# Kernel optimization log

Measured on AMD Instinct MI355X. Metric: run time of the kernel, lower is better.

## Reference

```python
import jax, jax.numpy as jnp
import numpy as np

S = 1.0   # scale s
M = 0.4   # margin m
EPS = 1e-12  # F.normalize eps


def _l2norm_rows(a):
    # F.normalize(a, dim=1): row-wise L2 normalization
    n = jnp.linalg.norm(a, axis=1, keepdims=True)
    return a / jnp.maximum(n, EPS)


def _half_loss(sim):
    # unique-label branch: positive is the diagonal, all off-diagonal are negatives
    N = sim.shape[0]
    num = S * (jnp.diagonal(sim) - M)                       # [N]
    offdiag = jnp.exp(S * sim) * (1.0 - jnp.eye(N, dtype=sim.dtype))
    denom = jnp.exp(num) + jnp.sum(offdiag, axis=1)         # [N]
    return num - jnp.log(denom)


def setup_inputs() -> dict:
    key = jax.random.key(0)
    k1, k2 = jax.random.split(key)
    N, D = 8192, 256
    return {
        "x1": jax.random.normal(k1, (N, D), dtype=jnp.float32),
        "x2": jax.random.normal(k2, (N, D), dtype=jnp.float32),
        "sentence_id": jnp.arange(N, dtype=jnp.int32),  # unique labels -> more_label=False branch
    }


def reference(x1, x2, sentence_id):
    # x12[i,j] row-normalized similarity of x1_i against all x2_j (and symmetric)
    x12 = _l2norm_rows(x1 @ x2.T)   # [N, N]
    x21 = _l2norm_rows(x2 @ x1.T)   # [N, N]
    L12 = _half_loss(x12)
    L21 = _half_loss(x21)
    loss = -jnp.mean(L12) - jnp.mean(L21)
    return loss, L12, L21
```

## Files before the change

kernel.cpp:

```cpp
#include <hip/hip_runtime.h>
#include <cstdint>
#include <cstddef>


#define NROWS 8192
#define DIMK 256
#define MARGIN 0.4f
#define LOG2E 1.4426950408889634f
#define LN2 0.6931471805599453f

typedef short short8 __attribute__((ext_vector_type(8)));
typedef float f32x4 __attribute__((ext_vector_type(4)));
typedef long longx2 __attribute__((ext_vector_type(2)));

__device__ __forceinline__ unsigned short f2bf(float f) {
  union { float f; unsigned u; } v; v.f = f;
  unsigned r = (v.u + 0x7fffu + ((v.u >> 16) & 1u)) >> 16;
  return (unsigned short)r;
}

__device__ __forceinline__ unsigned char f2fp8(float f) {
  union { float f; unsigned u; } v; v.f = f;
  const unsigned s = (v.u >> 24) & 0x80u;
  const unsigned au = v.u & 0x7fffffffu;
  if (au >= 0x43e00000u) return (unsigned char)(s | 0x7eu);
  int e = (int)(au >> 23) - 127;
  if (e >= -6) {
    unsigned mfull = (au & 0x7fffffu) | 0x800000u;
    unsigned r = (mfull + 0x7ffffu + ((mfull >> 20) & 1u)) >> 20;
    if (r == 16u) { r = 8u; ++e; }
    return (unsigned char)(s | ((unsigned)(e + 7) << 3) | (r & 7u));
  }
  float scaled = __builtin_fabsf(f) * 512.0f;
  unsigned n = (unsigned)(scaled + 0.5f);
  if (n >= 8u) return (unsigned char)(s | 0x08u);
  return (unsigned char)(s | n);
}

__device__ __forceinline__ void gl_lds16(const void* g, void* l) {
  __builtin_amdgcn_global_load_lds((const __attribute__((address_space(1))) void*)g,
                                   (__attribute__((address_space(3))) void*)l, 16, 0, 0);
}

__device__ __forceinline__ float fexp(float x) {
  return __builtin_amdgcn_exp2f(x * LOG2E);
}

__global__ __launch_bounds__(256)
void k_prep(const float* __restrict__ x1, const float* __restrict__ x2,
            unsigned short* __restrict__ Ab, unsigned short* __restrict__ Bb,
            unsigned char* __restrict__ A8, unsigned char* __restrict__ B8,
            float* __restrict__ diag, float* __restrict__ zero_region) {
  const int t = threadIdx.x;
  if (blockIdx.x < 2048) {
    const int row = blockIdx.x * 4 + (t >> 6);
    const int l = t & 63;
    const float4 a = ((const float4*)(x1 + (size_t)row * DIMK))[l];
    const float4 b = ((const float4*)(x2 + (size_t)row * DIMK))[l];
    ushort4 ua, ub;
    ua.x = f2bf(a.x); ua.y = f2bf(a.y); ua.z = f2bf(a.z); ua.w = f2bf(a.w);
    ub.x = f2bf(b.x); ub.y = f2bf(b.y); ub.z = f2bf(b.z); ub.w = f2bf(b.w);
    ((ushort4*)(Ab + (size_t)row * DIMK))[l] = ua;
    ((ushort4*)(Bb + (size_t)row * DIMK))[l] = ub;
    uchar4 qa, qb;
    qa.x = f2fp8(a.x); qa.y = f2fp8(a.y); qa.z = f2fp8(a.z); qa.w = f2fp8(a.w);
    qb.x = f2fp8(b.x); qb.y = f2fp8(b.y); qb.z = f2fp8(b.z); qb.w = f2fp8(b.w);
    ((uchar4*)(A8 + (size_t)row * DIMK))[l] = qa;
    ((uchar4*)(B8 + (size_t)row * DIMK))[l] = qb;
    float d = a.x * b.x + a.y * b.y + a.z * b.z + a.w * b.w;
#pragma unroll
    for (int m = 1; m < 64; m <<= 1) d += __shfl_xor(d, m);
    if (l == 0) diag[row] = d;
  } else {
    const size_t off = (size_t)(blockIdx.x - 2048) * 1024 + t * 4;
    float4 z = {0.f, 0.f, 0.f, 0.f};
    *(float4*)(zero_region + off) = z;
  }
}

__global__ __launch_bounds__(256)
void k_syrk(const unsigned short* __restrict__ Ab, const unsigned short* __restrict__ Bb,
            float* __restrict__ M1, float* __restrict__ M2) {
  __shared__ unsigned short As[64 * 32];
  __shared__ unsigned short Bs[64 * 32];
  const int t = threadIdx.x, w = t >> 6, l = t & 63, quad = l >> 4, l15 = l & 15;
  const int mat = blockIdx.z & 1;
  const int kseg = blockIdx.z >> 1;
  const unsigned short* X = mat ? Bb : Ab;
  float* Mo = mat ? M2 : M1;
  const int a0 = blockIdx.y * 64, b0 = blockIdx.x * 64;
  const int wr = (w >> 1) * 32, wc = (w & 1) * 32;
  f32x4 acc[2][2] = {};
  const int nn = t & 31, cb = t >> 5;
  const int c0 = cb * 8;
  const int nb = kseg * 256;
  for (int n0 = nb; n0 < nb + 256; n0 += 32) {
    short8 va = *(const short8*)(X + (size_t)(n0 + nn) * DIMK + a0 + c0);
    short8 vb = *(const short8*)(X + (size_t)(n0 + nn) * DIMK + b0 + c0);
#pragma unroll
    for (int i = 0; i < 8; ++i) {
      const int c = c0 + i;
      const int sl = (((nn >> 3) ^ ((c >> 1) & 3)) << 3) + (nn & 7);
      As[c * 32 + sl] = va[i];
      Bs[c * 32 + sl] = vb[i];
    }
    __syncthreads();
    short8 af[2], bg[2];
#pragma unroll
    for (int i = 0; i < 2; ++i) {
      const int ra = wr + i * 16 + l15;
      af[i] = *(const short8*)&As[ra * 32 + ((quad ^ ((ra >> 1) & 3)) << 3)];
      const int rb = wc + i * 16 + l15;
      bg[i] = *(const short8*)&Bs[rb * 32 + ((quad ^ ((rb >> 1) & 3)) << 3)];
    }
#pragma unroll
    for (int i = 0; i < 2; ++i)
#pragma unroll
      for (int j = 0; j < 2; ++j)
        acc[i][j] = __builtin_amdgcn_mfma_f32_16x16x32_bf16(af[i], bg[j], acc[i][j], 0, 0, 0);
    __syncthreads();
  }
#pragma unroll
  for (int i = 0; i < 2; ++i)
#pragma unroll
    for (int j = 0; j < 2; ++j)
#pragma unroll
      for (int r = 0; r < 4; ++r) {
        const int lr = wr + i * 16 + quad * 4 + r;
        const int lc = wc + j * 16 + l15;
        atomicAdd(&Mo[(size_t)(a0 + lr) * 256 + b0 + lc], acc[i][j][r]);
      }
}

__global__ __launch_bounds__(256)
void k_gemmN(const unsigned short* __restrict__ Ab, const unsigned short* __restrict__ Bb,
             const float* __restrict__ M1, const float* __restrict__ M2,
             const float* __restrict__ x1, const float* __restrict__ x2,
             float* __restrict__ rowsq, float* __restrict__ colsq) {
  __shared__ unsigned short As[2][4096];
  __shared__ unsigned short Bs[2][4096];
  const int t = threadIdx.x, w = t >> 6, l = t & 63, quad = l >> 4, l15 = l & 15;
  const unsigned short* A;
  const float* Mf;
  const float* Xf;
  float* sq;
  if ((blockIdx.z & 1) == 0) { A = Ab; Mf = M2; Xf = x1; sq = rowsq; }
  else                       { A = Bb; Mf = M1; Xf = x2; sq = colsq; }
  const int kbase = (blockIdx.z >> 1) * 128;
  const int row0 = blockIdx.x * 128;
  const int col0 = blockIdx.y * 128;
  const int wr = (w >> 1) * 64, wc = (w & 1) * 64;
  f32x4 acc[4][4] = {};

  const int sr0 = l >> 2, slot = l & 3;
  const int cA = w * 2, cB = w * 2 + 1;
  const int rA = cA * 16 + sr0, rB = cB * 16 + sr0;
  const int scA = (slot ^ ((rA >> 1) & 3)) << 3;
  const int scB = (slot ^ ((rB >> 1) & 3)) << 3;
  const unsigned short* pA0 = A + (size_t)(row0 + rA) * DIMK + kbase + scA;
  const unsigned short* pA1 = A + (size_t)(row0 + rB) * DIMK + kbase + scB;
  const int dA0 = cA * 512 + l * 8, dA1 = cB * 512 + l * 8;

  auto stageB = [&](int k0, int buf) {
#pragma unroll
    for (int g = 0; g < 2; ++g) {
      const int e = g * 2048 + t * 8;
      const int c = e >> 5, kk = e & 31;
      const float4 v0 = *(const float4*)(Mf + (size_t)(col0 + c) * 256 + kbase + k0 + kk);
      const float4 v1 = *(const float4*)(Mf + (size_t)(col0 + c) * 256 + kbase + k0 + kk + 4);
      ushort4 u0, u1;
      u0.x = f2bf(v0.x); u0.y = f2bf(v0.y); u0.z = f2bf(v0.z); u0.w = f2bf(v0.w);
      u1.x = f2bf(v1.x); u1.y = f2bf(v1.y); u1.z = f2bf(v1.z); u1.w = f2bf(v1.w);
      const int sw = ((kk >> 3) ^ ((c >> 1) & 3)) << 3;
      *(ushort4*)&Bs[buf][c * 32 + sw] = u0;
      *(ushort4*)&Bs[buf][c * 32 + sw + 4] = u1;
    }
  };
  auto issueA = [&](int k0, int buf) {
    gl_lds16(pA0 + k0, &As[buf][dA0]);
    gl_lds16(pA1 + k0, &As[buf][dA1]);
  };

  stageB(0, 0);
  issueA(0, 0);
#pragma unroll
  for (int k = 0; k < 4; ++k) {
    const int cur = k & 1;
    __syncthreads();
    if (k < 3) { stageB((k + 1) * 32, cur ^ 1); issueA((k + 1) * 32, cur ^ 1); }
    short8 af[4], bg[4];
#pragma unroll
    for (int i = 0; i < 4; ++i) {
      const int ra = wr + i * 16 + l15;
      af[i] = *(const short8*)&As[cur][ra * 32 + ((quad ^ ((ra >> 1) & 3)) << 3)];
      const int rb = wc + i * 16 + l15;
      bg[i] = *(const short8*)&Bs[cur][rb * 32 + ((quad ^ ((rb >> 1) & 3)) << 3)];
    }
#pragma unroll
    for (int i = 0; i < 4; ++i)
#pragma unroll
      for (int j = 0; j < 4; ++j)
        acc[i][j] = __builtin_amdgcn_mfma_f32_16x16x32_bf16(af[i], bg[j], acc[i][j], 0, 0, 0);
  }

#pragma unroll
  for (int i = 0; i < 4; ++i) {
#pragma unroll
    for (int r = 0; r < 4; ++r) {
      const int lr = wr + i * 16 + quad * 4 + r;
      const float* xr = Xf + (size_t)(row0 + lr) * DIMK + col0 + wc;
      float rp = 0.f;
#pragma unroll
      for (int j = 0; j < 4; ++j) rp += acc[i][j][r] * xr[j * 16 + l15];
      rp += __shfl_xor(rp, 1); rp += __shfl_xor(rp, 2);
      rp += __shfl_xor(rp, 4); rp += __shfl_xor(rp, 8);
      if (l15 == 0) atomicAdd(&sq[row0 + lr], rp);
    }
  }
}

__global__ __launch_bounds__(256)
void k_gemmE(const unsigned char* __restrict__ A8, const unsigned char* __restrict__ B8,
             const float* __restrict__ rowsq, const float* __restrict__ colsq,
             float* __restrict__ rowExp, float* __restrict__ colExp) {
  __shared__ unsigned char As[2][8192];
  __shared__ unsigned char Bs[2][8192];
  __shared__ float cRow[128];
  __shared__ float cCol[128];

  const int t = threadIdx.x;
  const int w = t >> 6;
  const int l = t & 63;
  const int quad = l >> 4;
  const int l15 = l & 15;
  const int row0 = blockIdx.x * 128;
  const int col0 = blockIdx.y * 128;
  const int wr = (w >> 1) * 64;
  const int wc = (w & 1) * 64;

  if (t < 128) cRow[t] = LOG2E * rsqrtf(rowsq[row0 + t]);
  else cCol[t - 128] = LOG2E * rsqrtf(colsq[col0 + t - 128]);

  f32x4 acc[4][4] = {};

  const int srow = t >> 2;
  const int cl = (t & 3) ^ ((t >> 3) & 3);
  const unsigned char* gA0 = A8 + (size_t)(row0 + srow) * DIMK + cl * 16;
  const unsigned char* gA1 = A8 + (size_t)(row0 + 64 + srow) * DIMK + cl * 16;
  const unsigned char* gB0 = B8 + (size_t)(col0 + srow) * DIMK + cl * 16;
  const unsigned char* gB1 = B8 + (size_t)(col0 + 64 + srow) * DIMK + cl * 16;
  const int d0 = t * 16, d1 = 4096 + t * 16;

  auto issue = [&](int k0, int buf) {
    gl_lds16(gA0 + k0, &As[buf][d0]);
    gl_lds16(gA1 + k0, &As[buf][d1]);
    gl_lds16(gB0 + k0, &Bs[buf][d0]);
    gl_lds16(gB1 + k0, &Bs[buf][d1]);
  };

  issue(0, 0);
#pragma unroll
  for (int it = 0; it < 4; ++it) {
    const int cur = it & 1;
    __syncthreads();
    if (it < 3) issue((it + 1) * 64, cur ^ 1);
    longx2 av[4], bv[4];
#pragma unroll
    for (int i = 0; i < 4; ++i) {
      const int ra = wr + i * 16 + l15;
      const int pcA = quad ^ ((ra >> 1) & 3);
      av[i] = *(const longx2*)&As[cur][ra * 64 + pcA * 16];
      const int rb = wc + i * 16 + l15;
      const int pcB = quad ^ ((rb >> 1) & 3);
      bv[i] = *(const longx2*)&Bs[cur][rb * 64 + pcB * 16];
    }
#pragma unroll
    for (int kc = 0; kc < 2; ++kc)
#pragma unroll
      for (int i = 0; i < 4; ++i)
#pragma unroll
        for (int j = 0; j < 4; ++j)
          acc[i][j] = __builtin_amdgcn_mfma_f32_16x16x32_fp8_fp8(av[i][kc], bv[j][kc],
                                                                 acc[i][j], 0, 0, 0);
  }

  float cj[4];
#pragma unroll
  for (int j = 0; j < 4; ++j) cj[j] = cCol[wc + j * 16 + l15];
  float colpart[4] = {0.f, 0.f, 0.f, 0.f};
#pragma unroll
  for (int i = 0; i < 4; ++i) {
#pragma unroll
    for (int r = 0; r < 4; ++r) {
      const int lr = wr + i * 16 + quad * 4 + r;
      const float ci = cRow[lr];
      float rp = 0.f;
#pragma unroll
      for (int j = 0; j < 4; ++j) {
        const float g = acc[i][j][r];
        rp += __builtin_amdgcn_exp2f(g * ci);
        colpart[j] += __builtin_amdgcn_exp2f(g * cj[j]);
      }
      rp += __shfl_xor(rp, 1); rp += __shfl_xor(rp, 2);
      rp += __shfl_xor(rp, 4); rp += __shfl_xor(rp, 8);
      if (l15 == 0) atomicAdd(&rowExp[row0 + lr], rp);
    }
  }
#pragma unroll
  for (int j = 0; j < 4; ++j) {
    float cp = colpart[j];
    cp += __shfl_xor(cp, 16); cp += __shfl_xor(cp, 32);
    if (l < 16) atomicAdd(&colExp[col0 + wc + j * 16 + l15], cp);
  }
}

__global__ __launch_bounds__(1024)
void k_final(const float* __restrict__ rowsq, const float* __restrict__ colsq,
             const float* __restrict__ diag, const float* __restrict__ rowExp,
             const float* __restrict__ colExp, float* __restrict__ out,
             double* __restrict__ lossAcc, int* __restrict__ doneCnt) {
  const int t = threadIdx.x;
  const int i = blockIdx.x * 1024 + t;
  const float d = diag[i];
  const float s1 = d * rsqrtf(rowsq[i]);
  const float s2 = d * rsqrtf(colsq[i]);
  const float n1 = s1 - MARGIN, n2 = s2 - MARGIN;
  const float L1 = n1 - LN2 * __builtin_amdgcn_logf(rowExp[i] - fexp(s1) + fexp(n1));
  const float L2 = n2 - LN2 * __builtin_amdgcn_logf(colExp[i] - fexp(s2) + fexp(n2));
  out[1 + i] = L1;
  out[1 + NROWS + i] = L2;
  double part = (double)L1 + (double)L2;
#pragma unroll
  for (int m = 1; m < 64; m <<= 1) part += __shfl_xor(part, m);
  __shared__ double red[16];
  if ((t & 63) == 0) red[t >> 6] = part;
  __syncthreads();
  if (t == 0) {
    double s = 0.0;
#pragma unroll
    for (int q = 0; q < 16; ++q) s += red[q];
    atomicAdd(lossAcc, s);
    __threadfence();
    if (atomicAdd(doneCnt, 1) == 7) {
      const double la =
          __hip_atomic_load(lossAcc, __ATOMIC_ACQUIRE, __HIP_MEMORY_SCOPE_AGENT);
      out[0] = (float)(-la / (double)NROWS);
    }
  }
}

extern "C" void kernel_launch(void* const* d_in, const int* in_sizes, int n_in,
                              void* d_out, int out_size, void* d_ws, size_t ws_size,
                              hipStream_t stream) {
  const float* x1 = (const float*)d_in[0];
  const float* x2 = (const float*)d_in[1];
  float* out = (float*)d_out;
  char* ws = (char*)d_ws;

  unsigned short* Ab = (unsigned short*)(ws);
  unsigned short* Bb = (unsigned short*)(ws + 4194304);
  float* M1 = (float*)(ws + 8388608);
  float* M2 = (float*)(ws + 8650752);
  float* rowsq = (float*)(ws + 8912896);
  float* colsq = (float*)(ws + 8945664);
  float* rowExp = (float*)(ws + 8978432);
  float* colExp = (float*)(ws + 9011200);
  char* ctrl = ws + 9043968;
  double* lossAcc = (double*)(ctrl);
  int* doneCnt = (int*)(ctrl + 256);
  float* diag = (float*)(ws + 9048064);
  unsigned char* A8 = (unsigned char*)(ws + 9080832);
  unsigned char* B8 = (unsigned char*)(ws + 11177984);

  k_prep<<<2209, 256, 0, stream>>>(x1, x2, Ab, Bb, A8, B8, diag,
                                   (float*)(ws + 8388608));
  k_syrk<<<dim3(4, 4, 64), 256, 0, stream>>>(Ab, Bb, M1, M2);
  k_gemmN<<<dim3(64, 2, 4), 256, 0, stream>>>(Ab, Bb, M1, M2, x1, x2, rowsq, colsq);
  k_gemmE<<<dim3(64, 64), 256, 0, stream>>>(A8, B8, rowsq, colsq, rowExp, colExp);
  k_final<<<8, 1024, 0, stream>>>(rowsq, colsq, diag, rowExp, colExp, out,
                                  lossAcc, doneCnt);
}
```

Before: 170.9 us.

## Fuse all five kernels into one persistent cooperative kernel with grid syncs

Merges the prep, SYRK, norm GEMM, fp8 exp GEMM and final reduction kernels into a single cooperative persistent kernel. Each phase loops over virtual block indices, and grid-wide syncs separate the phases, which removes four kernel launch boundaries and the done-counter handshake. The trade-offs are a shared LDS footprint sized for the largest phase, which may reduce occupancy, plus grid.sync costs and less latency hiding in the GEMM phases when the grid is capped at the number of resident blocks.

```diff
diff --git a/kernel.cpp b/kernel.cpp
--- a/kernel.cpp
+++ b/kernel.cpp
@@ -1,4 +1,5 @@
 #include <hip/hip_runtime.h>
+#include <hip/hip_cooperative_groups.h>
 #include <cstdint>
 #include <cstddef>
 
@@ -8,6 +9,8 @@
 #define MARGIN 0.4f
 #define LOG2E 1.4426950408889634f
 #define LN2 0.6931471805599453f
+
+namespace cg = cooperative_groups;
 
 typedef short short8 __attribute__((ext_vector_type(8)));
 typedef float f32x4 __attribute__((ext_vector_type(4)));
@@ -47,305 +50,304 @@
 }
 
 __global__ __launch_bounds__(256)
-void k_prep(const float* __restrict__ x1, const float* __restrict__ x2,
+void k_mega(const float* __restrict__ x1, const float* __restrict__ x2,
             unsigned short* __restrict__ Ab, unsigned short* __restrict__ Bb,
             unsigned char* __restrict__ A8, unsigned char* __restrict__ B8,
-            float* __restrict__ diag, float* __restrict__ zero_region) {
+            float* __restrict__ zero_region,
+            float* __restrict__ M1, float* __restrict__ M2,
+            float* __restrict__ rowsq, float* __restrict__ colsq,
+            float* __restrict__ rowExp, float* __restrict__ colExp,
+            float* __restrict__ diag, double* __restrict__ lossAcc,
+            float* __restrict__ out) {
+  __shared__ __align__(16) char smem[33792];
+  cg::grid_group gg = cg::this_grid();
   const int t = threadIdx.x;
-  if (blockIdx.x < 2048) {
-    const int row = blockIdx.x * 4 + (t >> 6);
-    const int l = t & 63;
-    const float4 a = ((const float4*)(x1 + (size_t)row * DIMK))[l];
-    const float4 b = ((const float4*)(x2 + (size_t)row * DIMK))[l];
-    ushort4 ua, ub;
-    ua.x = f2bf(a.x); ua.y = f2bf(a.y); ua.z = f2bf(a.z); ua.w = f2bf(a.w);
-    ub.x = f2bf(b.x); ub.y = f2bf(b.y); ub.z = f2bf(b.z); ub.w = f2bf(b.w);
-    ((ushort4*)(Ab + (size_t)row * DIMK))[l] = ua;
-    ((ushort4*)(Bb + (size_t)row * DIMK))[l] = ub;
-    uchar4 qa, qb;
-    qa.x = f2fp8(a.x); qa.y = f2fp8(a.y); qa.z = f2fp8(a.z); qa.w = f2fp8(a.w);
-    qb.x = f2fp8(b.x); qb.y = f2fp8(b.y); qb.z = f2fp8(b.z); qb.w = f2fp8(b.w);
-    ((uchar4*)(A8 + (size_t)row * DIMK))[l] = qa;
-    ((uchar4*)(B8 + (size_t)row * DIMK))[l] = qb;
-    float d = a.x * b.x + a.y * b.y + a.z * b.z + a.w * b.w;
-#pragma unroll
-    for (int m = 1; m < 64; m <<= 1) d += __shfl_xor(d, m);
-    if (l == 0) diag[row] = d;
-  } else {
-    const size_t off = (size_t)(blockIdx.x - 2048) * 1024 + t * 4;
-    float4 z = {0.f, 0.f, 0.f, 0.f};
-    *(float4*)(zero_region + off) = z;
-  }
-}
-
-__global__ __launch_bounds__(256)
-void k_syrk(const unsigned short* __restrict__ Ab, const unsigned short* __restrict__ Bb,
-            float* __restrict__ M1, float* __restrict__ M2) {
-  __shared__ unsigned short As[64 * 32];
-  __shared__ unsigned short Bs[64 * 32];
-  const int t = threadIdx.x, w = t >> 6, l = t & 63, quad = l >> 4, l15 = l & 15;
-  const int mat = blockIdx.z & 1;
-  const int kseg = blockIdx.z >> 1;
-  const unsigned short* X = mat ? Bb : Ab;
-  float* Mo = mat ? M2 : M1;
-  const int a0 = blockIdx.y * 64, b0 = blockIdx.x * 64;
-  const int wr = (w >> 1) * 32, wc = (w & 1) * 32;
-  f32x4 acc[2][2] = {};
-  const int nn = t & 31, cb = t >> 5;
-  const int c0 = cb * 8;
-  const int nb = kseg * 256;
-  for (int n0 = nb; n0 < nb + 256; n0 += 32) {
-    short8 va = *(const short8*)(X + (size_t)(n0 + nn) * DIMK + a0 + c0);
-    short8 vb = *(const short8*)(X + (size_t)(n0 + nn) * DIMK + b0 + c0);
-#pragma unroll
-    for (int i = 0; i < 8; ++i) {
-      const int c = c0 + i;
-      const int sl = (((nn >> 3) ^ ((c >> 1) & 3)) << 3) + (nn & 7);
-      As[c * 32 + sl] = va[i];
-      Bs[c * 32 + sl] = vb[i];
-    }
+  const int w = t >> 6, l = t & 63, quad = l >> 4, l15 = l & 15;
+
+  for (int v = blockIdx.x; v < 2209; v += gridDim.x) {
+    if (v < 2048) {
+      const int row = v * 4 + w;
+      const float4 a = ((const float4*)(x1 + (size_t)row * DIMK))[l];
+      const float4 b = ((const float4*)(x2 + (size_t)row * DIMK))[l];
+      ushort4 ua, ub;
+      ua.x = f2bf(a.x); ua.y = f2bf(a.y); ua.z = f2bf(a.z); ua.w = f2bf(a.w);
+      ub.x = f2bf(b.x); ub.y = f2bf(b.y); ub.z = f2bf(b.z); ub.w = f2bf(b.w);
+      ((ushort4*)(Ab + (size_t)row * DIMK))[l] = ua;
+      ((ushort4*)(Bb + (size_t)row * DIMK))[l] = ub;
+      uchar4 qa, qb;
+      qa.x = f2fp8(a.x); qa.y = f2fp8(a.y); qa.z = f2fp8(a.z); qa.w = f2fp8(a.w);
+      qb.x = f2fp8(b.x); qb.y = f2fp8(b.y); qb.z = f2fp8(b.z); qb.w = f2fp8(b.w);
+      ((uchar4*)(A8 + (size_t)row * DIMK))[l] = qa;
+      ((uchar4*)(B8 + (size_t)row * DIMK))[l] = qb;
+      float d = a.x * b.x + a.y * b.y + a.z * b.z + a.w * b.w;
+#pragma unroll
+      for (int m = 1; m < 64; m <<= 1) d += __shfl_xor(d, m);
+      if (l == 0) diag[row] = d;
+    } else {
+      const size_t off = (size_t)(v - 2048) * 1024 + t * 4;
+      float4 z = {0.f, 0.f, 0.f, 0.f};
+      *(float4*)(zero_region + off) = z;
+    }
+  }
+  gg.sync();
+
+  {
+    unsigned short* AsS = (unsigned short*)smem;
+    unsigned short* BsS = (unsigned short*)(smem + 8192);
+    const int wrS = (w >> 1) * 32, wcS = (w & 1) * 32;
+    const int nn = t & 31, c0 = (t >> 5) * 8;
+    for (int v = blockIdx.x; v < 1024; v += gridDim.x) {
+      __syncthreads();
+      const int bxS = v & 3, byS = (v >> 2) & 3, bzS = v >> 4;
+      const int mat = bzS & 1, kseg = bzS >> 1;
+      const unsigned short* X = mat ? Bb : Ab;
+      float* Mo = mat ? M2 : M1;
+      const int a0 = byS * 64, b0 = bxS * 64;
+      f32x4 acc[2][2] = {};
+      const int nb = kseg * 256;
+      for (int n0 = nb; n0 < nb + 256; n0 += 32) {
+        short8 va = *(const short8*)(X + (size_t)(n0 + nn) * DIMK + a0 + c0);
+        short8 vb = *(const short8*)(X + (size_t)(n0 + nn) * DIMK + b0 + c0);
+#pragma unroll
+        for (int i = 0; i < 8; ++i) {
+          const int c = c0 + i;
+          const int sl = (((nn >> 3) ^ ((c >> 1) & 3)) << 3) + (nn & 7);
+          AsS[c * 32 + sl] = va[i];
+          BsS[c * 32 + sl] = vb[i];
+        }
+        __syncthreads();
+        short8 af[2], bg[2];
+#pragma unroll
+        for (int i = 0; i < 2; ++i) {
+          const int ra = wrS + i * 16 + l15;
+          af[i] = *(const short8*)&AsS[ra * 32 + ((quad ^ ((ra >> 1) & 3)) << 3)];
+          const int rb = wcS + i * 16 + l15;
+          bg[i] = *(const short8*)&BsS[rb * 32 + ((quad ^ ((rb >> 1) & 3)) << 3)];
+        }
+#pragma unroll
+        for (int i = 0; i < 2; ++i)
+#pragma unroll
+          for (int j = 0; j < 2; ++j)
+            acc[i][j] = __builtin_amdgcn_mfma_f32_16x16x32_bf16(af[i], bg[j], acc[i][j], 0, 0, 0);
+        __syncthreads();
+      }
+#pragma unroll
+      for (int i = 0; i < 2; ++i)
+#pragma unroll
+        for (int j = 0; j < 2; ++j)
+#pragma unroll
+          for (int r = 0; r < 4; ++r) {
+            const int lr = wrS + i * 16 + quad * 4 + r;
+            const int lc = wcS + j * 16 + l15;
+            atomicAdd(&Mo[(size_t)(a0 + lr) * 256 + b0 + lc], acc[i][j][r]);
+          }
+    }
+  }
+  gg.sync();
+
+  {
+    unsigned short* AsN = (unsigned short*)smem;
+    unsigned short* BsN = (unsigned short*)(smem + 16384);
+    const int wrN = (w >> 1) * 64, wcN = (w & 1) * 64;
+    const int sr0 = l >> 2, slot = l & 3;
+    for (int v = blockIdx.x; v < 512; v += gridDim.x) {
+      __syncthreads();
+      const int bxN = v & 63, byN = (v >> 6) & 1, bzN = v >> 7;
+      const unsigned short* A;
+      const float* Mf;
+      const float* Xf;
+      float* sq;
+      if ((bzN & 1) == 0) { A = Ab; Mf = M2; Xf = x1; sq = rowsq; }
+      else                { A = Bb; Mf = M1; Xf = x2; sq = colsq; }
+      const int kbase = (bzN >> 1) * 128;
+      const int row0 = bxN * 128;
+      const int col0 = byN * 128;
+      f32x4 acc[4][4] = {};
+
+      const int cA = w * 2, cB = w * 2 + 1;
+      const int rA = cA * 16 + sr0, rB = cB * 16 + sr0;
+      const int scA = (slot ^ ((rA >> 1) & 3)) << 3;
+      const int scB = (slot ^ ((rB >> 1) & 3)) << 3;
+      const unsigned short* pA0 = A + (size_t)(row0 + rA) * DIMK + kbase + scA;
+      const unsigned short* pA1 = A + (size_t)(row0 + rB) * DIMK + kbase + scB;
+      const int dA0 = cA * 512 + l * 8, dA1 = cB * 512 + l * 8;
+
+      auto stageB = [&](int k0, int buf) {
+#pragma unroll
+        for (int g = 0; g < 2; ++g) {
+          const int e = g * 2048 + t * 8;
+          const int c = e >> 5, kk = e & 31;
+          const float4 v0 = *(const float4*)(Mf + (size_t)(col0 + c) * 256 + kbase + k0 + kk);
+          const float4 v1 = *(const float4*)(Mf + (size_t)(col0 + c) * 256 + kbase + k0 + kk + 4);
+          ushort4 u0, u1;
+          u0.x = f2bf(v0.x); u0.y = f2bf(v0.y); u0.z = f2bf(v0.z); u0.w = f2bf(v0.w);
+          u1.x = f2bf(v1.x); u1.y = f2bf(v1.y); u1.z = f2bf(v1.z); u1.w = f2bf(v1.w);
+          const int sw = ((kk >> 3) ^ ((c >> 1) & 3)) << 3;
+          *(ushort4*)&BsN[buf * 4096 + c * 32 + sw] = u0;
+          *(ushort4*)&BsN[buf * 4096 + c * 32 + sw + 4] = u1;
+        }
+      };
+      auto issueA = [&](int k0, int buf) {
+        gl_lds16(pA0 + k0, &AsN[buf * 4096 + dA0]);
+        gl_lds16(pA1 + k0, &AsN[buf * 4096 + dA1]);
+      };
+
+      stageB(0, 0);
+      issueA(0, 0);
+#pragma unroll
+      for (int k = 0; k < 4; ++k) {
+        const int cur = k & 1;
+        __syncthreads();
+        if (k < 3) { stageB((k + 1) * 32, cur ^ 1); issueA((k + 1) * 32, cur ^ 1); }
+        short8 af[4], bg[4];
+#pragma unroll
+        for (int i = 0; i < 4; ++i) {
+          const int ra = wrN + i * 16 + l15;
+          af[i] = *(const short8*)&AsN[cur * 4096 + ra * 32 + ((quad ^ ((ra >> 1) & 3)) << 3)];
+          const int rb = wcN + i * 16 + l15;
+          bg[i] = *(const short8*)&BsN[cur * 4096 + rb * 32 + ((quad ^ ((rb >> 1) & 3)) << 3)];
+        }
+#pragma unroll
+        for (int i = 0; i < 4; ++i)
+#pragma unroll
+          for (int j = 0; j < 4; ++j)
+            acc[i][j] = __builtin_amdgcn_mfma_f32_16x16x32_bf16(af[i], bg[j], acc[i][j], 0, 0, 0);
+      }
+
+#pragma unroll
+      for (int i = 0; i < 4; ++i) {
+#pragma unroll
+        for (int r = 0; r < 4; ++r) {
+          const int lr = wrN + i * 16 + quad * 4 + r;
+          const float* xr = Xf + (size_t)(row0 + lr) * DIMK + col0 + wcN;
+          float rp = 0.f;
+#pragma unroll
+          for (int j = 0; j < 4; ++j) rp += acc[i][j][r] * xr[j * 16 + l15];
+          rp += __shfl_xor(rp, 1); rp += __shfl_xor(rp, 2);
+          rp += __shfl_xor(rp, 4); rp += __shfl_xor(rp, 8);
+          if (l15 == 0) atomicAdd(&sq[row0 + lr], rp);
+        }
+      }
+    }
+  }
+  gg.sync();
+
+  {
+    unsigned char* AsE = (unsigned char*)smem;
+    unsigned char* BsE = (unsigned char*)(smem + 16384);
+    float* cRow = (float*)(smem + 32768);
+    float* cCol = (float*)(smem + 33280);
+    const int wrE = (w >> 1) * 64, wcE = (w & 1) * 64;
+    const int srow = t >> 2;
+    const int cl = (t & 3) ^ ((t >> 3) & 3);
+    const int d0 = t * 16, d1 = 4096 + t * 16;
+    for (int v = blockIdx.x; v < 4096; v += gridDim.x) {
+      __syncthreads();
+      const int row0 = (v & 63) * 128;
+      const int col0 = (v >> 6) * 128;
+      if (t < 128) cRow[t] = LOG2E * rsqrtf(rowsq[row0 + t]);
+      else cCol[t - 128] = LOG2E * rsqrtf(colsq[col0 + t - 128]);
+
+      f32x4 acc[4][4] = {};
+      const unsigned char* gA0 = A8 + (size_t)(row0 + srow) * DIMK + cl * 16;
+      const unsigned char* gA1 = A8 + (size_t)(row0 + 64 + srow) * DIMK + cl * 16;
+      const unsigned char* gB0 = B8 + (size_t)(col0 + srow) * DIMK + cl * 16;
+      const unsigned char* gB1 = B8 + (size_t)(col0 + 64 + srow) * DIMK + cl * 16;
+
+      auto issue = [&](int k0, int buf) {
+        gl_lds16(gA0 + k0, &AsE[buf * 8192 + d0]);
+        gl_lds16(gA1 + k0, &AsE[buf * 8192 + d1]);
+        gl_lds16(gB0 + k0, &BsE[buf * 8192 + d0]);
+        gl_lds16(gB1 + k0, &BsE[buf * 8192 + d1]);
+      };
+
+      issue(0, 0);
+#pragma unroll
+      for (int it = 0; it < 4; ++it) {
+        const int cur = it & 1;
+        __syncthreads();
+        if (it < 3) issue((it + 1) * 64, cur ^ 1);
+        longx2 av[4], bv[4];
+#pragma unroll
+        for (int i = 0; i < 4; ++i) {
+          const int ra = wrE + i * 16 + l15;
+          const int pcA = quad ^ ((ra >> 1) & 3);
+          av[i] = *(const longx2*)&AsE[cur * 8192 + ra * 64 + pcA * 16];
+          const int rb = wcE + i * 16 + l15;
+          const int pcB = quad ^ ((rb >> 1) & 3);
+          bv[i] = *(const longx2*)&BsE[cur * 8192 + rb * 64 + pcB * 16];
+        }
+#pragma unroll
+        for (int kc = 0; kc < 2; ++kc)
+#pragma unroll
+          for (int i = 0; i < 4; ++i)
+#pragma unroll
+            for (int j = 0; j < 4; ++j)
+              acc[i][j] = __builtin_amdgcn_mfma_f32_16x16x32_fp8_fp8(av[i][kc], bv[j][kc],
+                                                                     acc[i][j], 0, 0, 0);
+      }
+
+      float cj[4];
+#pragma unroll
+      for (int j = 0; j < 4; ++j) cj[j] = cCol[wcE + j * 16 + l15];
+      float colpart[4] = {0.f, 0.f, 0.f, 0.f};
+#pragma unroll
+      for (int i = 0; i < 4; ++i) {
+#pragma unroll
+        for (int r = 0; r < 4; ++r) {
+          const int lr = wrE + i * 16 + quad * 4 + r;
+          const float ci = cRow[lr];
+          float rp = 0.f;
+#pragma unroll
+          for (int j = 0; j < 4; ++j) {
+            const float g = acc[i][j][r];
+            rp += __builtin_amdgcn_exp2f(g * ci);
+            colpart[j] += __builtin_amdgcn_exp2f(g * cj[j]);
+          }
+          rp += __shfl_xor(rp, 1); rp += __shfl_xor(rp, 2);
+          rp += __shfl_xor(rp, 4); rp += __shfl_xor(rp, 8);
+          if (l15 == 0) atomicAdd(&rowExp[row0 + lr], rp);
+        }
+      }
+#pragma unroll
+      for (int j = 0; j < 4; ++j) {
+        float cp = colpart[j];
+        cp += __shfl_xor(cp, 16); cp += __shfl_xor(cp, 32);
+        if (l < 16) atomicAdd(&colExp[col0 + wcE + j * 16 + l15], cp);
+      }
+    }
+  }
+  gg.sync();
+
+  {
+    double part = 0.0;
+    for (int v = blockIdx.x; v < 32; v += gridDim.x) {
+      const int i = v * 256 + t;
+      const float d = diag[i];
+      const float s1 = d * rsqrtf(rowsq[i]);
+      const float s2 = d * rsqrtf(colsq[i]);
+      const float n1 = s1 - MARGIN, n2 = s2 - MARGIN;
+      const float L1 = n1 - LN2 * __builtin_amdgcn_logf(rowExp[i] - fexp(s1) + fexp(n1));
+      const float L2 = n2 - LN2 * __builtin_amdgcn_logf(colExp[i] - fexp(s2) + fexp(n2));
+      out[1 + i] = L1;
+      out[1 + NROWS + i] = L2;
+      part += (double)L1 + (double)L2;
+    }
+#pragma unroll
+    for (int m = 1; m < 64; m <<= 1) part += __shfl_xor(part, m);
+    double* red = (double*)smem;
     __syncthreads();
-    short8 af[2], bg[2];
-#pragma unroll
-    for (int i = 0; i < 2; ++i) {
-      const int ra = wr + i * 16 + l15;
-      af[i] = *(const short8*)&As[ra * 32 + ((quad ^ ((ra >> 1) & 3)) << 3)];
-      const int rb = wc + i * 16 + l15;
-      bg[i] = *(const short8*)&Bs[rb * 32 + ((quad ^ ((rb >> 1) & 3)) << 3)];
-    }
-#pragma unroll
-    for (int i = 0; i < 2; ++i)
-#pragma unroll
-      for (int j = 0; j < 2; ++j)
-        acc[i][j] = __builtin_amdgcn_mfma_f32_16x16x32_bf16(af[i], bg[j], acc[i][j], 0, 0, 0);
+    if (l == 0) red[w] = part;
     __syncthreads();
-  }
-#pragma unroll
-  for (int i = 0; i < 2; ++i)
-#pragma unroll
-    for (int j = 0; j < 2; ++j)
-#pragma unroll
-      for (int r = 0; r < 4; ++r) {
-        const int lr = wr + i * 16 + quad * 4 + r;
-        const int lc = wc + j * 16 + l15;
-        atomicAdd(&Mo[(size_t)(a0 + lr) * 256 + b0 + lc], acc[i][j][r]);
-      }
-}
-
-__global__ __launch_bounds__(256)
-void k_gemmN(const unsigned short* __restrict__ Ab, const unsigned short* __restrict__ Bb,
-             const float* __restrict__ M1, const float* __restrict__ M2,
-             const float* __restrict__ x1, const float* __restrict__ x2,
-             float* __restrict__ rowsq, float* __restrict__ colsq) {
-  __shared__ unsigned short As[2][4096];
-  __shared__ unsigned short Bs[2][4096];
-  const int t = threadIdx.x, w = t >> 6, l = t & 63, quad = l >> 4, l15 = l & 15;
-  const unsigned short* A;
-  const float* Mf;
-  const float* Xf;
-  float* sq;
-  if ((blockIdx.z & 1) == 0) { A = Ab; Mf = M2; Xf = x1; sq = rowsq; }
-  else                       { A = Bb; Mf = M1; Xf = x2; sq = colsq; }
-  const int kbase = (blockIdx.z >> 1) * 128;
-  const int row0 = blockIdx.x * 128;
-  const int col0 = blockIdx.y * 128;
-  const int wr = (w >> 1) * 64, wc = (w & 1) * 64;
-  f32x4 acc[4][4] = {};
-
-  const int sr0 = l >> 2, slot = l & 3;
-  const int cA = w * 2, cB = w * 2 + 1;
-  const int rA = cA * 16 + sr0, rB = cB * 16 + sr0;
-  const int scA = (slot ^ ((rA >> 1) & 3)) << 3;
-  const int scB = (slot ^ ((rB >> 1) & 3)) << 3;
-  const unsigned short* pA0 = A + (size_t)(row0 + rA) * DIMK + kbase + scA;
-  const unsigned short* pA1 = A + (size_t)(row0 + rB) * DIMK + kbase + scB;
-  const int dA0 = cA * 512 + l * 8, dA1 = cB * 512 + l * 8;
-
-  auto stageB = [&](int k0, int buf) {
-#pragma unroll
-    for (int g = 0; g < 2; ++g) {
-      const int e = g * 2048 + t * 8;
-      const int c = e >> 5, kk = e & 31;
-      const float4 v0 = *(const float4*)(Mf + (size_t)(col0 + c) * 256 + kbase + k0 + kk);
-      const float4 v1 = *(const float4*)(Mf + (size_t)(col0 + c) * 256 + kbase + k0 + kk + 4);
-      ushort4 u0, u1;
-      u0.x = f2bf(v0.x); u0.y = f2bf(v0.y); u0.z = f2bf(v0.z); u0.w = f2bf(v0.w);
-      u1.x = f2bf(v1.x); u1.y = f2bf(v1.y); u1.z = f2bf(v1.z); u1.w = f2bf(v1.w);
-      const int sw = ((kk >> 3) ^ ((c >> 1) & 3)) << 3;
-      *(ushort4*)&Bs[buf][c * 32 + sw] = u0;
-      *(ushort4*)&Bs[buf][c * 32 + sw + 4] = u1;
-    }
-  };
-  auto issueA = [&](int k0, int buf) {
-    gl_lds16(pA0 + k0, &As[buf][dA0]);
-    gl_lds16(pA1 + k0, &As[buf][dA1]);
-  };
-
-  stageB(0, 0);
-  issueA(0, 0);
-#pragma unroll
-  for (int k = 0; k < 4; ++k) {
-    const int cur = k & 1;
-    __syncthreads();
-    if (k < 3) { stageB((k + 1) * 32, cur ^ 1); issueA((k + 1) * 32, cur ^ 1); }
-    short8 af[4], bg[4];
-#pragma unroll
-    for (int i = 0; i < 4; ++i) {
-      const int ra = wr + i * 16 + l15;
-      af[i] = *(const short8*)&As[cur][ra * 32 + ((quad ^ ((ra >> 1) & 3)) << 3)];
-      const int rb = wc + i * 16 + l15;
-      bg[i] = *(const short8*)&Bs[cur][rb * 32 + ((quad ^ ((rb >> 1) & 3)) << 3)];
-    }
-#pragma unroll
-    for (int i = 0; i < 4; ++i)
-#pragma unroll
-      for (int j = 0; j < 4; ++j)
-        acc[i][j] = __builtin_amdgcn_mfma_f32_16x16x32_bf16(af[i], bg[j], acc[i][j], 0, 0, 0);
-  }
-
-#pragma unroll
-  for (int i = 0; i < 4; ++i) {
-#pragma unroll
-    for (int r = 0; r < 4; ++r) {
-      const int lr = wr + i * 16 + quad * 4 + r;
-      const float* xr = Xf + (size_t)(row0 + lr) * DIMK + col0 + wc;
-      float rp = 0.f;
-#pragma unroll
-      for (int j = 0; j < 4; ++j) rp += acc[i][j][r] * xr[j * 16 + l15];
-      rp += __shfl_xor(rp, 1); rp += __shfl_xor(rp, 2);
-      rp += __shfl_xor(rp, 4); rp += __shfl_xor(rp, 8);
-      if (l15 == 0) atomicAdd(&sq[row0 + lr], rp);
-    }
-  }
-}
-
-__global__ __launch_bounds__(256)
-void k_gemmE(const unsigned char* __restrict__ A8, const unsigned char* __restrict__ B8,
-             const float* __restrict__ rowsq, const float* __restrict__ colsq,
-             float* __restrict__ rowExp, float* __restrict__ colExp) {
-  __shared__ unsigned char As[2][8192];
-  __shared__ unsigned char Bs[2][8192];
-  __shared__ float cRow[128];
-  __shared__ float cCol[128];
-
-  const int t = threadIdx.x;
-  const int w = t >> 6;
-  const int l = t & 63;
-  const int quad = l >> 4;
-  const int l15 = l & 15;
-  const int row0 = blockIdx.x * 128;
-  const int col0 = blockIdx.y * 128;
-  const int wr = (w >> 1) * 64;
-  const int wc = (w & 1) * 64;
-
-  if (t < 128) cRow[t] = LOG2E * rsqrtf(rowsq[row0 + t]);
-  else cCol[t - 128] = LOG2E * rsqrtf(colsq[col0 + t - 128]);
-
-  f32x4 acc[4][4] = {};
-
-  const int srow = t >> 2;
-  const int cl = (t & 3) ^ ((t >> 3) & 3);
-  const unsigned char* gA0 = A8 + (size_t)(row0 + srow) * DIMK + cl * 16;
-  const unsigned char* gA1 = A8 + (size_t)(row0 + 64 + srow) * DIMK + cl * 16;
-  const unsigned char* gB0 = B8 + (size_t)(col0 + srow) * DIMK + cl * 16;
-  const unsigned char* gB1 = B8 + (size_t)(col0 + 64 + srow) * DIMK + cl * 16;
-  const int d0 = t * 16, d1 = 4096 + t * 16;
-
-  auto issue = [&](int k0, int buf) {
-    gl_lds16(gA0 + k0, &As[buf][d0]);
-    gl_lds16(gA1 + k0, &As[buf][d1]);
-    gl_lds16(gB0 + k0, &Bs[buf][d0]);
-    gl_lds16(gB1 + k0, &Bs[buf][d1]);
-  };
-
-  issue(0, 0);
-#pragma unroll
-  for (int it = 0; it < 4; ++it) {
-    const int cur = it & 1;
-    __syncthreads();
-    if (it < 3) issue((it + 1) * 64, cur ^ 1);
-    longx2 av[4], bv[4];
-#pragma unroll
-    for (int i = 0; i < 4; ++i) {
-      const int ra = wr + i * 16 + l15;
-      const int pcA = quad ^ ((ra >> 1) & 3);
-      av[i] = *(const longx2*)&As[cur][ra * 64 + pcA * 16];
-      const int rb = wc + i * 16 + l15;
-      const int pcB = quad ^ ((rb >> 1) & 3);
-      bv[i] = *(const longx2*)&Bs[cur][rb * 64 + pcB * 16];
-    }
-#pragma unroll
-    for (int kc = 0; kc < 2; ++kc)
-#pragma unroll
-      for (int i = 0; i < 4; ++i)
-#pragma unroll
-        for (int j = 0; j < 4; ++j)
-          acc[i][j] = __builtin_amdgcn_mfma_f32_16x16x32_fp8_fp8(av[i][kc], bv[j][kc],
-                                                                 acc[i][j], 0, 0, 0);
-  }
-
-  float cj[4];
-#pragma unroll
-  for (int j = 0; j < 4; ++j) cj[j] = cCol[wc + j * 16 + l15];
-  float colpart[4] = {0.f, 0.f, 0.f, 0.f};
-#pragma unroll
-  for (int i = 0; i < 4; ++i) {
-#pragma unroll
-    for (int r = 0; r < 4; ++r) {
-      const int lr = wr + i * 16 + quad * 4 + r;
-      const float ci = cRow[lr];
-      float rp = 0.f;
-#pragma unroll
-      for (int j = 0; j < 4; ++j) {
-        const float g = acc[i][j][r];
-        rp += __builtin_amdgcn_exp2f(g * ci);
-        colpart[j] += __builtin_amdgcn_exp2f(g * cj[j]);
-      }
-      rp += __shfl_xor(rp, 1); rp += __shfl_xor(rp, 2);
-      rp += __shfl_xor(rp, 4); rp += __shfl_xor(rp, 8);
-      if (l15 == 0) atomicAdd(&rowExp[row0 + lr], rp);
-    }
-  }
-#pragma unroll
-  for (int j = 0; j < 4; ++j) {
-    float cp = colpart[j];
-    cp += __shfl_xor(cp, 16); cp += __shfl_xor(cp, 32);
-    if (l < 16) atomicAdd(&colExp[col0 + wc + j * 16 + l15], cp);
-  }
-}
-
-__global__ __launch_bounds__(1024)
-void k_final(const float* __restrict__ rowsq, const float* __restrict__ colsq,
-             const float* __restrict__ diag, const float* __restrict__ rowExp,
-             const float* __restrict__ colExp, float* __restrict__ out,
-             double* __restrict__ lossAcc, int* __restrict__ doneCnt) {
-  const int t = threadIdx.x;
-  const int i = blockIdx.x * 1024 + t;
-  const float d = diag[i];
-  const float s1 = d * rsqrtf(rowsq[i]);
-  const float s2 = d * rsqrtf(colsq[i]);
-  const float n1 = s1 - MARGIN, n2 = s2 - MARGIN;
-  const float L1 = n1 - LN2 * __builtin_amdgcn_logf(rowExp[i] - fexp(s1) + fexp(n1));
-  const float L2 = n2 - LN2 * __builtin_amdgcn_logf(colExp[i] - fexp(s2) + fexp(n2));
-  out[1 + i] = L1;
-  out[1 + NROWS + i] = L2;
-  double part = (double)L1 + (double)L2;
-#pragma unroll
-  for (int m = 1; m < 64; m <<= 1) part += __shfl_xor(part, m);
-  __shared__ double red[16];
-  if ((t & 63) == 0) red[t >> 6] = part;
-  __syncthreads();
-  if (t == 0) {
-    double s = 0.0;
-#pragma unroll
-    for (int q = 0; q < 16; ++q) s += red[q];
-    atomicAdd(lossAcc, s);
-    __threadfence();
-    if (atomicAdd(doneCnt, 1) == 7) {
-      const double la =
-          __hip_atomic_load(lossAcc, __ATOMIC_ACQUIRE, __HIP_MEMORY_SCOPE_AGENT);
-      out[0] = (float)(-la / (double)NROWS);
-    }
+    if (t == 0) {
+      const double s = red[0] + red[1] + red[2] + red[3];
+      if (s != 0.0) atomicAdd(lossAcc, s);
+    }
+  }
+  gg.sync();
+  if (blockIdx.x == 0 && t == 0) {
+    const double la = __hip_atomic_load(lossAcc, __ATOMIC_RELAXED, __HIP_MEMORY_SCOPE_AGENT);
+    out[0] = (float)(-la / (double)NROWS);
   }
 }
 
@@ -359,6 +361,7 @@
 
   unsigned short* Ab = (unsigned short*)(ws);
   unsigned short* Bb = (unsigned short*)(ws + 4194304);
+  float* zr = (float*)(ws + 8388608);
   float* M1 = (float*)(ws + 8388608);
   float* M2 = (float*)(ws + 8650752);
   float* rowsq = (float*)(ws + 8912896);
@@ -367,16 +370,19 @@
   float* colExp = (float*)(ws + 9011200);
   char* ctrl = ws + 9043968;
   double* lossAcc = (double*)(ctrl);
-  int* doneCnt = (int*)(ctrl + 256);
   float* diag = (float*)(ws + 9048064);
   unsigned char* A8 = (unsigned char*)(ws + 9080832);
   unsigned char* B8 = (unsigned char*)(ws + 11177984);
 
-  k_prep<<<2209, 256, 0, stream>>>(x1, x2, Ab, Bb, A8, B8, diag,
-                                   (float*)(ws + 8388608));
-  k_syrk<<<dim3(4, 4, 64), 256, 0, stream>>>(Ab, Bb, M1, M2);
-  k_gemmN<<<dim3(64, 2, 4), 256, 0, stream>>>(Ab, Bb, M1, M2, x1, x2, rowsq, colsq);
-  k_gemmE<<<dim3(64, 64), 256, 0, stream>>>(A8, B8, rowsq, colsq, rowExp, colExp);
-  k_final<<<8, 1024, 0, stream>>>(rowsq, colsq, diag, rowExp, colExp, out,
-                                  lossAcc, doneCnt);
-}
+  int maxB = 0;
+  hipOccupancyMaxActiveBlocksPerMultiprocessor(&maxB, k_mega, 256, 0);
+  if (maxB < 1) maxB = 1;
+  unsigned grid = (unsigned)maxB * 256u;
+  if (grid > 4096u) grid = 4096u;
+
+  void* args[] = {(void*)&x1, (void*)&x2, (void*)&Ab, (void*)&Bb,
+                  (void*)&A8, (void*)&B8, (void*)&zr, (void*)&M1, (void*)&M2,
+                  (void*)&rowsq, (void*)&colsq, (void*)&rowExp, (void*)&colExp,
+                  (void*)&diag, (void*)&lossAcc, (void*)&out};
+  hipLaunchCooperativeKernel((void*)k_mega, dim3(grid), dim3(256), args, 0, stream);
+}
```

Measured after the change: 379.3 us. +122.0%, slower.
